# Kernel optimization log

Hardware: AMD Instinct MI355X
Metric: run time of the kernel (lower is better)

## Reference

```python
import jax, jax.numpy as jnp
import numpy as np

B, S, D = 4, 2048, 768   # batch, seq_len, dim_inp
H, E = 12, 64            # num_heads, dim_out (per-head)
LN_EPS = 1e-5


def setup_inputs() -> dict:
    key = jax.random.key(0)
    ks = jax.random.split(key, 12)
    sd = 1.0 / np.sqrt(D)
    x = jax.random.normal(ks[0], (B, S, D), dtype=jnp.float32)
    Wq = jax.random.normal(ks[1], (H, D, E), dtype=jnp.float32) * sd
    bq = jax.random.normal(ks[2], (H, E), dtype=jnp.float32) * 0.02
    Wk = jax.random.normal(ks[3], (H, D, E), dtype=jnp.float32) * sd
    bk = jax.random.normal(ks[4], (H, E), dtype=jnp.float32) * 0.02
    Wv = jax.random.normal(ks[5], (H, D, E), dtype=jnp.float32) * sd
    bv = jax.random.normal(ks[6], (H, E), dtype=jnp.float32) * 0.02
    Wo = jax.random.normal(ks[7], (H * E, D), dtype=jnp.float32) * (1.0 / np.sqrt(H * E))
    bo = jax.random.normal(ks[8], (D,), dtype=jnp.float32) * 0.02
    gamma = jnp.ones((D,), dtype=jnp.float32)
    beta = jnp.zeros((D,), dtype=jnp.float32)
    return {"input_tensor": x, "Wq": Wq, "bq": bq, "Wk": Wk, "bk": bk,
            "Wv": Wv, "bv": bv, "Wo": Wo, "bo": bo, "gamma": gamma, "beta": beta}


def reference(input_tensor, Wq, bq, Wk, bk, Wv, bv, Wo, bo, gamma, beta):
    x = input_tensor  # [B,S,D]
    # all heads at once: [B,H,S,E]
    q = jnp.einsum('bsd,hde->bhse', x, Wq) + bq[None, :, None, :]
    k = jnp.einsum('bsd,hde->bhse', x, Wk) + bk[None, :, None, :]
    v = jnp.einsum('bsd,hde->bhse', x, Wv) + bv[None, :, None, :]
    # NOTE: original divides by sqrt(seq_len) (query.size(1)), not sqrt(head_dim)
    scale = jnp.sqrt(jnp.float32(q.shape[2]))
    scores = jnp.einsum('bhse,bhte->bhst', q, k) / scale  # [B,H,S,S]
    attn = jax.nn.softmax(scores, axis=-1)
    ctx = jnp.einsum('bhst,bhte->bhse', attn, v)          # [B,H,S,E]
    # concat heads along last dim: [B,S,H*E]
    ctx = ctx.transpose(0, 2, 1, 3).reshape(x.shape[0], x.shape[1], -1)
    proj = ctx @ Wo + bo                                   # [B,S,D]
    h = x + proj
    mu = jnp.mean(h, axis=-1, keepdims=True)
    var = jnp.mean(jnp.square(h - mu), axis=-1, keepdims=True)
    y = (h - mu) * jax.lax.rsqrt(var + LN_EPS) * gamma + beta
    return y
```

## Files before the change

### kernel.cpp

```cpp
#include <hip/hip_runtime.h>


typedef __bf16 bf16x8 __attribute__((ext_vector_type(8)));
typedef __bf16 bf16x4 __attribute__((ext_vector_type(4)));
typedef float  f32x4  __attribute__((ext_vector_type(4)));

#define MFMA16(a,b,c) __builtin_amdgcn_mfma_f32_16x16x32_bf16((a),(b),(c),0,0,0)
#define QSCALE2 (0.022097086912079612f * 1.4426950408889634f)

__device__ __forceinline__ void gload16(const void* g, void* l) {
  __builtin_amdgcn_global_load_lds((const __attribute__((address_space(1))) void*)g,
                                   (__attribute__((address_space(3))) void*)l, 16, 0, 0);
}

__global__ __launch_bounds__(256) void pack_kernel(
    const float* __restrict__ x, const float* __restrict__ Wq,
    const float* __restrict__ Wk, const float* __restrict__ Wv,
    const float* __restrict__ Wo,
    __bf16* __restrict__ xb, __bf16* __restrict__ wqkv, __bf16* __restrict__ wot) {
  int tid = blockIdx.x * 256 + threadIdx.x;
  int nth = gridDim.x * 256;
  for (int i = tid; i < 8192 * 768 / 4; i += nth) {
    float4 v = ((const float4*)x)[i];
    bf16x4 o; o[0] = (__bf16)v.x; o[1] = (__bf16)v.y; o[2] = (__bf16)v.z; o[3] = (__bf16)v.w;
    ((bf16x4*)xb)[i] = o;
  }
  for (int i = tid; i < 3 * 768 * 768; i += nth) {
    int n = i / 768, d = i - n * 768;
    int p = n / 768;
    int wn = n - p * 768;
    int h = wn >> 6, e = wn & 63;
    const float* W = (p == 0) ? Wq : (p == 1) ? Wk : Wv;
    wqkv[i] = (__bf16)W[(h * 768 + d) * 64 + e];
  }
  for (int i = tid; i < 768 * 768; i += nth) {
    int n = i / 768, k = i - n * 768;
    wot[i] = (__bf16)Wo[k * 768 + n];
  }
}

#define GEMM_CORE(A_, Bt_, m0_, n0_)                                              \
  __shared__ __bf16 As[128 * 32];                                                 \
  __shared__ __bf16 Bs[128 * 32];                                                 \
  const int tid = threadIdx.x;                                                    \
  const int w = tid >> 6, lane = tid & 63, ln = lane & 15, hi = lane >> 4;        \
  const int wr = w >> 1, wc = w & 1;                                              \
  f32x4 acc[4][4];                                                                \
  {                                                                               \
    f32x4 z = {0.f, 0.f, 0.f, 0.f};                                               \
    _Pragma("unroll") for (int i = 0; i < 4; ++i)                                 \
      _Pragma("unroll") for (int j = 0; j < 4; ++j) acc[i][j] = z;                \
  }                                                                               \
  {                                                                               \
    const int r0 = tid >> 2, cc = (tid & 3) * 8;                                  \
    const __bf16* ga0 = A_ + (size_t)(m0_ + r0) * 768 + cc;                       \
    const __bf16* ga1 = A_ + (size_t)(m0_ + 64 + r0) * 768 + cc;                  \
    const __bf16* gb0 = Bt_ + (size_t)(n0_ + r0) * 768 + cc;                      \
    const __bf16* gb1 = Bt_ + (size_t)(n0_ + 64 + r0) * 768 + cc;                 \
    __bf16* la0 = &As[w * 512];                                                   \
    __bf16* la1 = &As[2048 + w * 512];                                            \
    __bf16* lb0 = &Bs[w * 512];                                                   \
    __bf16* lb1 = &Bs[2048 + w * 512];                                            \
    for (int kt = 0; kt < 24; ++kt) {                                             \
      const int kk = kt * 32;                                                     \
      gload16(ga0 + kk, la0);                                                     \
      gload16(ga1 + kk, la1);                                                     \
      gload16(gb0 + kk, lb0);                                                     \
      gload16(gb1 + kk, lb1);                                                     \
      __syncthreads();                                                            \
      bf16x8 af[4], bfv[4];                                                       \
      _Pragma("unroll") for (int mt = 0; mt < 4; ++mt)                            \
        af[mt] = *(const bf16x8*)&As[(wr * 64 + mt * 16 + ln) * 32 + hi * 8];     \
      _Pragma("unroll") for (int nt = 0; nt < 4; ++nt)                            \
        bfv[nt] = *(const bf16x8*)&Bs[(wc * 64 + nt * 16 + ln) * 32 + hi * 8];    \
      _Pragma("unroll") for (int mt = 0; mt < 4; ++mt)                            \
        _Pragma("unroll") for (int nt = 0; nt < 4; ++nt)                          \
          acc[mt][nt] = MFMA16(af[mt], bfv[nt], acc[mt][nt]);                     \
      __syncthreads();                                                            \
    }                                                                             \
  }

__global__ __launch_bounds__(256) void gemm_qkv(
    const __bf16* __restrict__ A, const __bf16* __restrict__ Bt,
    const float* __restrict__ bq, const float* __restrict__ bk,
    const float* __restrict__ bv,
    __bf16* __restrict__ qb, __bf16* __restrict__ kb, __bf16* __restrict__ vt) {
  const int m0 = blockIdx.y * 128, n0 = blockIdx.x * 128;
  GEMM_CORE(A, Bt, m0, n0)
  const int p = n0 / 768;
  const float* bias = (p == 0) ? bq : (p == 1) ? bk : bv;
  const float sc = (p == 0) ? QSCALE2 : 1.0f;
#pragma unroll
  for (int nt = 0; nt < 4; ++nt) {
    int n = n0 + wc * 64 + nt * 16 + ln;
    int wn = n - p * 768;
    int h = wn >> 6, e = wn & 63;
    float bb = bias[wn];
#pragma unroll
    for (int mt = 0; mt < 4; ++mt) {
      int mrow = m0 + wr * 64 + mt * 16 + hi * 4;
      int b = mrow >> 11, s0 = mrow & 2047;
      if (p == 2) {
        bf16x4 pk;
#pragma unroll
        for (int r = 0; r < 4; ++r) pk[r] = (__bf16)(acc[mt][nt][r] + bb);
        *(bf16x4*)&vt[(((size_t)b * 12 + h) * 64 + e) * 2048 + s0] = pk;
      } else {
        __bf16* dst = (p == 0) ? qb : kb;
#pragma unroll
        for (int r = 0; r < 4; ++r)
          dst[(((size_t)b * 12 + h) * 2048 + s0 + r) * 64 + e] =
              (__bf16)((acc[mt][nt][r] + bb) * sc);
      }
    }
  }
}

__global__ __launch_bounds__(256) void gemm_proj(
    const __bf16* __restrict__ A, const __bf16* __restrict__ Bt,
    const float* __restrict__ bo, const float* __restrict__ xres,
    float* __restrict__ hout) {
  const int m0 = blockIdx.y * 128, n0 = blockIdx.x * 128;
  GEMM_CORE(A, Bt, m0, n0)
#pragma unroll
  for (int nt = 0; nt < 4; ++nt) {
    int n = n0 + wc * 64 + nt * 16 + ln;
    float bb = bo[n];
#pragma unroll
    for (int mt = 0; mt < 4; ++mt) {
      int mrow = m0 + wr * 64 + mt * 16 + hi * 4;
#pragma unroll
      for (int r = 0; r < 4; ++r) {
        size_t idx = (size_t)(mrow + r) * 768 + n;
        hout[idx] = acc[mt][nt][r] + bb + xres[idx];
      }
    }
  }
}

__global__ __launch_bounds__(256) void attn_kernel(
    const __bf16* __restrict__ qb, const __bf16* __restrict__ kb,
    const __bf16* __restrict__ vt, __bf16* __restrict__ ctx) {
  __shared__ __bf16 Kl[64 * 72];
  __shared__ __bf16 Vl[64 * 72];
  __shared__ __bf16 Pl[4][16 * 72];
  const int tid = threadIdx.x;
  const int w = tid >> 6, lane = tid & 63, ln = lane & 15, hi = lane >> 4;
  const int bh = blockIdx.x;
  const int q0 = blockIdx.y * 64;

  const __bf16* qrow = qb + ((size_t)bh * 2048 + q0 + w * 16 + ln) * 64;
  bf16x8 qf0 = *(const bf16x8*)(qrow + hi * 8);
  bf16x8 qf1 = *(const bf16x8*)(qrow + 32 + hi * 8);

  float lsum = 0.f;
  f32x4 cacc[4];
  {
    f32x4 z = {0.f, 0.f, 0.f, 0.f};
#pragma unroll
    for (int eg = 0; eg < 4; ++eg) cacc[eg] = z;
  }

  const int sr = tid >> 3, sc = (tid & 7) * 8;
  const __bf16* gk = kb + ((size_t)bh * 2048 + sr) * 64 + sc;
  const __bf16* gv = vt + ((size_t)bh * 64 + sr) * 2048 + sc;

  bf16x8 k0 = *(const bf16x8*)(gk);
  bf16x8 k1 = *(const bf16x8*)(gk + 32 * 64);
  bf16x8 v0 = *(const bf16x8*)(gv);
  bf16x8 v1 = *(const bf16x8*)(gv + 32 * 2048);

  for (int t = 0; t < 32; ++t) {
    __syncthreads();
    *(bf16x8*)&Kl[sr * 72 + sc] = k0;
    *(bf16x8*)&Kl[(sr + 32) * 72 + sc] = k1;
    *(bf16x8*)&Vl[sr * 72 + sc] = v0;
    *(bf16x8*)&Vl[(sr + 32) * 72 + sc] = v1;
    __syncthreads();
    if (t < 31) {
      const __bf16* nk = gk + (size_t)(t + 1) * 64 * 64;
      const __bf16* nv = gv + (size_t)(t + 1) * 64;
      k0 = *(const bf16x8*)(nk);
      k1 = *(const bf16x8*)(nk + 32 * 64);
      v0 = *(const bf16x8*)(nv);
      v1 = *(const bf16x8*)(nv + 32 * 2048);
    }
#pragma unroll
    for (int tq = 0; tq < 4; ++tq) {
      bf16x8 ka = *(const bf16x8*)&Kl[(tq * 16 + ln) * 72 + hi * 8];
      bf16x8 kb2 = *(const bf16x8*)&Kl[(tq * 16 + ln) * 72 + 32 + hi * 8];
      f32x4 z = {0.f, 0.f, 0.f, 0.f};
      z = MFMA16(ka, qf0, z);
      z = MFMA16(kb2, qf1, z);
      bf16x4 pk;
#pragma unroll
      for (int r = 0; r < 4; ++r) {
        float p = __builtin_amdgcn_exp2f(z[r]);
        lsum += p;
        pk[r] = (__bf16)p;
      }
      *(bf16x4*)&Pl[w][ln * 72 + tq * 16 + hi * 4] = pk;
    }
    bf16x8 pa0 = *(const bf16x8*)&Pl[w][ln * 72 + hi * 8];
    bf16x8 pa1 = *(const bf16x8*)&Pl[w][ln * 72 + 32 + hi * 8];
#pragma unroll
    for (int eg = 0; eg < 4; ++eg) {
      bf16x8 bv0 = *(const bf16x8*)&Vl[(eg * 16 + ln) * 72 + hi * 8];
      bf16x8 bv1 = *(const bf16x8*)&Vl[(eg * 16 + ln) * 72 + 32 + hi * 8];
      cacc[eg] = MFMA16(pa0, bv0, cacc[eg]);
      cacc[eg] = MFMA16(pa1, bv1, cacc[eg]);
    }
  }
  lsum += __shfl_xor(lsum, 16, 64);
  lsum += __shfl_xor(lsum, 32, 64);
  const int b = bh / 12, h = bh - b * 12;
#pragma unroll
  for (int r = 0; r < 4; ++r) {
    float lq = __shfl(lsum, (lane & 48) + hi * 4 + r, 64);
    float rl = 1.0f / lq;
    int qr = q0 + w * 16 + hi * 4 + r;
#pragma unroll
    for (int eg = 0; eg < 4; ++eg)
      ctx[((size_t)b * 2048 + qr) * 768 + h * 64 + eg * 16 + ln] =
          (__bf16)(cacc[eg][r] * rl);
  }
}

__global__ __launch_bounds__(256) void ln_kernel(
    const float* __restrict__ hb, const float* __restrict__ gamma,
    const float* __restrict__ beta, float* __restrict__ out) {
  __shared__ float ssum[4], ssq[4];
  const int row = blockIdx.x, t = threadIdx.x;
  const float* hr = hb + (size_t)row * 768;
  float v0 = hr[t], v1 = hr[t + 256], v2 = hr[t + 512];
  float sum = v0 + v1 + v2;
  float sq = v0 * v0 + v1 * v1 + v2 * v2;
#pragma unroll
  for (int mask = 1; mask < 64; mask <<= 1) {
    sum += __shfl_xor(sum, mask, 64);
    sq += __shfl_xor(sq, mask, 64);
  }
  const int w = t >> 6;
  if ((t & 63) == 0) { ssum[w] = sum; ssq[w] = sq; }
  __syncthreads();
  float s1 = ssum[0] + ssum[1] + ssum[2] + ssum[3];
  float s2 = ssq[0] + ssq[1] + ssq[2] + ssq[3];
  float mu = s1 * (1.0f / 768.0f);
  float var = s2 * (1.0f / 768.0f) - mu * mu;
  float rs = rsqrtf(var + 1e-5f);
  float* orow = out + (size_t)row * 768;
  orow[t]       = (v0 - mu) * rs * gamma[t]       + beta[t];
  orow[t + 256] = (v1 - mu) * rs * gamma[t + 256] + beta[t + 256];
  orow[t + 512] = (v2 - mu) * rs * gamma[t + 512] + beta[t + 512];
}

extern "C" void kernel_launch(void* const* d_in, const int* in_sizes, int n_in,
                              void* d_out, int out_size, void* d_ws, size_t ws_size,
                              hipStream_t stream) {
  const float* x     = (const float*)d_in[0];
  const float* Wq    = (const float*)d_in[1];
  const float* bq    = (const float*)d_in[2];
  const float* Wk    = (const float*)d_in[3];
  const float* bk    = (const float*)d_in[4];
  const float* Wv    = (const float*)d_in[5];
  const float* bv    = (const float*)d_in[6];
  const float* Wo    = (const float*)d_in[7];
  const float* bo    = (const float*)d_in[8];
  const float* gamma = (const float*)d_in[9];
  const float* beta  = (const float*)d_in[10];
  float* out = (float*)d_out;

  char* ws = (char*)d_ws;
  __bf16* xb   = (__bf16*)(ws);
  __bf16* wqkv = (__bf16*)(ws + 12582912);
  __bf16* wot  = (__bf16*)(ws + 16121856);
  __bf16* qb   = (__bf16*)(ws + 17301504);
  __bf16* kb   = (__bf16*)(ws + 29884416);
  __bf16* vt   = (__bf16*)(ws + 42467328);
  __bf16* ctx  = (__bf16*)(ws + 55050240);
  float*  hb   = (float*)(ws + 67633152);

  pack_kernel<<<dim3(1024), dim3(256), 0, stream>>>(x, Wq, Wk, Wv, Wo, xb, wqkv, wot);
  gemm_qkv<<<dim3(18, 64), dim3(256), 0, stream>>>(xb, wqkv, bq, bk, bv, qb, kb, vt);
  attn_kernel<<<dim3(48, 32), dim3(256), 0, stream>>>(qb, kb, vt, ctx);
  gemm_proj<<<dim3(6, 64), dim3(256), 0, stream>>>(ctx, wot, bo, x, hb);
  ln_kernel<<<dim3(8192), dim3(256), 0, stream>>>(hb, gamma, beta, out);
}
```

Before: 194.3 us.

## Rework attention kernel with 32x32 MFMA, async double-buffered LDS, and register P

Rewrites the attention inner loop so each wave handles 32 query rows using 32x32x16 bf16 MFMAs, which halves the grid. K/V tiles are loaded straight into XOR-swizzled LDS with global_load_lds and double-buffered, so one barrier per iteration replaces two. The probability tile stays in registers through cvt_pk_bf16 and permlane32_swap instead of a round trip through LDS. Risks are higher register pressure and fewer blocks per CU, which could lower occupancy.

```diff
diff --git a/kernel.cpp b/kernel.cpp
--- a/kernel.cpp
+++ b/kernel.cpp
@@ -4,8 +4,11 @@
 typedef __bf16 bf16x8 __attribute__((ext_vector_type(8)));
 typedef __bf16 bf16x4 __attribute__((ext_vector_type(4)));
 typedef float  f32x4  __attribute__((ext_vector_type(4)));
+typedef float  f32x16 __attribute__((ext_vector_type(16)));
+typedef unsigned u32x4 __attribute__((ext_vector_type(4)));
 
 #define MFMA16(a,b,c) __builtin_amdgcn_mfma_f32_16x16x32_bf16((a),(b),(c),0,0,0)
+#define MFMA32(a,b,c) __builtin_amdgcn_mfma_f32_32x32x16_bf16((a),(b),(c),0,0,0)
 #define QSCALE2 (0.022097086912079612f * 1.4426950408889634f)
 
 __device__ __forceinline__ void gload16(const void* g, void* l) {
@@ -141,88 +144,114 @@
 __global__ __launch_bounds__(256) void attn_kernel(
     const __bf16* __restrict__ qb, const __bf16* __restrict__ kb,
     const __bf16* __restrict__ vt, __bf16* __restrict__ ctx) {
-  __shared__ __bf16 Kl[64 * 72];
-  __shared__ __bf16 Vl[64 * 72];
-  __shared__ __bf16 Pl[4][16 * 72];
+  __shared__ __align__(16) char lds[32768];
   const int tid = threadIdx.x;
-  const int w = tid >> 6, lane = tid & 63, ln = lane & 15, hi = lane >> 4;
+  const int w = tid >> 6, lane = tid & 63;
+  const int l31 = lane & 31, h = lane >> 5;
   const int bh = blockIdx.x;
-  const int q0 = blockIdx.y * 64;
-
-  const __bf16* qrow = qb + ((size_t)bh * 2048 + q0 + w * 16 + ln) * 64;
-  bf16x8 qf0 = *(const bf16x8*)(qrow + hi * 8);
-  bf16x8 qf1 = *(const bf16x8*)(qrow + 32 + hi * 8);
+  const int q0 = blockIdx.y * 128 + w * 32;
+
+  const int o0 = tid * 16, o1 = o0 + 4096;
+  const int r0s = o0 >> 7, cb0 = o0 & 127;
+  const int r1s = o1 >> 7, cb1 = o1 & 127;
+  const char* kgb = (const char*)(kb + (size_t)bh * 2048 * 64);
+  const char* vgb = (const char*)(vt + (size_t)bh * 64 * 2048);
+  const char* ksrc0 = kgb + r0s * 128 + (cb0 ^ ((r0s & 7) << 4));
+  const char* ksrc1 = kgb + r1s * 128 + (cb1 ^ ((r1s & 7) << 4));
+  const char* vsrc0 = vgb + r0s * 4096 + (cb0 ^ ((r0s & 7) << 4));
+  const char* vsrc1 = vgb + r1s * 4096 + (cb1 ^ ((r1s & 7) << 4));
+  char* kl0 = lds + w * 1024;
+  char* vl0 = lds + 16384 + w * 1024;
+
+#define STAGE(t_, b_) do {                                   \
+    gload16(ksrc0 + (size_t)(t_) * 8192, kl0 + (b_) * 8192); \
+    gload16(ksrc1 + (size_t)(t_) * 8192, kl0 + (b_) * 8192 + 4096); \
+    gload16(vsrc0 + (size_t)(t_) * 128,  vl0 + (b_) * 8192); \
+    gload16(vsrc1 + (size_t)(t_) * 128,  vl0 + (b_) * 8192 + 4096); \
+  } while (0)
+
+  const __bf16* qp = qb + ((size_t)bh * 2048 + q0 + l31) * 64 + h * 8;
+  bf16x8 qf[4];
+#pragma unroll
+  for (int s = 0; s < 4; ++s) qf[s] = *(const bf16x8*)(qp + 16 * s);
+
+  const int swz = (l31 & 7) << 4;
+  const int krd = l31 * 128 + ((h * 16) ^ swz);
+  const int vrd = 16384 + l31 * 128 + ((h * 16) ^ swz);
 
   float lsum = 0.f;
-  f32x4 cacc[4];
-  {
-    f32x4 z = {0.f, 0.f, 0.f, 0.f};
-#pragma unroll
-    for (int eg = 0; eg < 4; ++eg) cacc[eg] = z;
-  }
-
-  const int sr = tid >> 3, sc = (tid & 7) * 8;
-  const __bf16* gk = kb + ((size_t)bh * 2048 + sr) * 64 + sc;
-  const __bf16* gv = vt + ((size_t)bh * 64 + sr) * 2048 + sc;
-
-  bf16x8 k0 = *(const bf16x8*)(gk);
-  bf16x8 k1 = *(const bf16x8*)(gk + 32 * 64);
-  bf16x8 v0 = *(const bf16x8*)(gv);
-  bf16x8 v1 = *(const bf16x8*)(gv + 32 * 2048);
+  f32x16 cacc[2];
+#pragma unroll
+  for (int et = 0; et < 2; ++et)
+#pragma unroll
+    for (int r = 0; r < 16; ++r) cacc[et][r] = 0.f;
+
+  STAGE(0, 0);
+  __syncthreads();
+  int buf = 0;
 
   for (int t = 0; t < 32; ++t) {
+    if (t < 31) STAGE(t + 1, buf ^ 1);
+    const char* kb_l = lds + buf * 8192;
+    u32x4 pau[4];
+#pragma unroll
+    for (int kvt = 0; kvt < 2; ++kvt) {
+      f32x16 sa;
+#pragma unroll
+      for (int r = 0; r < 16; ++r) sa[r] = 0.f;
+      __builtin_amdgcn_s_setprio(1);
+#pragma unroll
+      for (int s = 0; s < 4; ++s) {
+        bf16x8 ka = *(const bf16x8*)(kb_l + ((krd + kvt * 4096) ^ (s * 32)));
+        sa = MFMA32(ka, qf[s], sa);
+      }
+      __builtin_amdgcn_s_setprio(0);
+      unsigned c0, c1, c2, c3, c4, c5, c6, c7;
+#define PKPAIR(dst_, i_)                                                     \
+      {                                                                      \
+        float pa_ = __builtin_amdgcn_exp2f(sa[2 * (i_)]);                    \
+        float pb_ = __builtin_amdgcn_exp2f(sa[2 * (i_) + 1]);                \
+        lsum += pa_ + pb_;                                                   \
+        asm("v_cvt_pk_bf16_f32 %0, %1, %2" : "=v"(dst_) : "v"(pa_), "v"(pb_)); \
+      }
+      PKPAIR(c0, 0) PKPAIR(c1, 1) PKPAIR(c2, 2) PKPAIR(c3, 3)
+      PKPAIR(c4, 4) PKPAIR(c5, 5) PKPAIR(c6, 6) PKPAIR(c7, 7)
+#undef PKPAIR
+      asm("v_permlane32_swap_b32 %0, %1" : "+v"(c0), "+v"(c2));
+      asm("v_permlane32_swap_b32 %0, %1" : "+v"(c1), "+v"(c3));
+      asm("v_permlane32_swap_b32 %0, %1" : "+v"(c4), "+v"(c6));
+      asm("v_permlane32_swap_b32 %0, %1" : "+v"(c5), "+v"(c7));
+      pau[2 * kvt][0] = c0; pau[2 * kvt][1] = c1;
+      pau[2 * kvt][2] = c2; pau[2 * kvt][3] = c3;
+      pau[2 * kvt + 1][0] = c4; pau[2 * kvt + 1][1] = c5;
+      pau[2 * kvt + 1][2] = c6; pau[2 * kvt + 1][3] = c7;
+    }
+    const char* vb_l = lds + buf * 8192;
+    __builtin_amdgcn_s_setprio(1);
+#pragma unroll
+    for (int ks = 0; ks < 4; ++ks) {
+      bf16x8 paf = __builtin_bit_cast(bf16x8, pau[ks]);
+      bf16x8 bv0 = *(const bf16x8*)(vb_l + ((vrd + 0 * 4096) ^ (ks * 32)));
+      bf16x8 bv1 = *(const bf16x8*)(vb_l + ((vrd + 1 * 4096) ^ (ks * 32)));
+      cacc[0] = MFMA32(paf, bv0, cacc[0]);
+      cacc[1] = MFMA32(paf, bv1, cacc[1]);
+    }
+    __builtin_amdgcn_s_setprio(0);
     __syncthreads();
-    *(bf16x8*)&Kl[sr * 72 + sc] = k0;
-    *(bf16x8*)&Kl[(sr + 32) * 72 + sc] = k1;
-    *(bf16x8*)&Vl[sr * 72 + sc] = v0;
-    *(bf16x8*)&Vl[(sr + 32) * 72 + sc] = v1;
-    __syncthreads();
-    if (t < 31) {
-      const __bf16* nk = gk + (size_t)(t + 1) * 64 * 64;
-      const __bf16* nv = gv + (size_t)(t + 1) * 64;
-      k0 = *(const bf16x8*)(nk);
-      k1 = *(const bf16x8*)(nk + 32 * 64);
-      v0 = *(const bf16x8*)(nv);
-      v1 = *(const bf16x8*)(nv + 32 * 2048);
-    }
-#pragma unroll
-    for (int tq = 0; tq < 4; ++tq) {
-      bf16x8 ka = *(const bf16x8*)&Kl[(tq * 16 + ln) * 72 + hi * 8];
-      bf16x8 kb2 = *(const bf16x8*)&Kl[(tq * 16 + ln) * 72 + 32 + hi * 8];
-      f32x4 z = {0.f, 0.f, 0.f, 0.f};
-      z = MFMA16(ka, qf0, z);
-      z = MFMA16(kb2, qf1, z);
-      bf16x4 pk;
-#pragma unroll
-      for (int r = 0; r < 4; ++r) {
-        float p = __builtin_amdgcn_exp2f(z[r]);
-        lsum += p;
-        pk[r] = (__bf16)p;
-      }
-      *(bf16x4*)&Pl[w][ln * 72 + tq * 16 + hi * 4] = pk;
-    }
-    bf16x8 pa0 = *(const bf16x8*)&Pl[w][ln * 72 + hi * 8];
-    bf16x8 pa1 = *(const bf16x8*)&Pl[w][ln * 72 + 32 + hi * 8];
-#pragma unroll
-    for (int eg = 0; eg < 4; ++eg) {
-      bf16x8 bv0 = *(const bf16x8*)&Vl[(eg * 16 + ln) * 72 + hi * 8];
-      bf16x8 bv1 = *(const bf16x8*)&Vl[(eg * 16 + ln) * 72 + 32 + hi * 8];
-      cacc[eg] = MFMA16(pa0, bv0, cacc[eg]);
-      cacc[eg] = MFMA16(pa1, bv1, cacc[eg]);
-    }
-  }
-  lsum += __shfl_xor(lsum, 16, 64);
+    buf ^= 1;
+  }
+#undef STAGE
+
   lsum += __shfl_xor(lsum, 32, 64);
-  const int b = bh / 12, h = bh - b * 12;
-#pragma unroll
-  for (int r = 0; r < 4; ++r) {
-    float lq = __shfl(lsum, (lane & 48) + hi * 4 + r, 64);
-    float rl = 1.0f / lq;
-    int qr = q0 + w * 16 + hi * 4 + r;
-#pragma unroll
-    for (int eg = 0; eg < 4; ++eg)
-      ctx[((size_t)b * 2048 + qr) * 768 + h * 64 + eg * 16 + ln] =
-          (__bf16)(cacc[eg][r] * rl);
+  float inv = 1.0f / lsum;
+  const int b = bh / 12, hh = bh - b * 12;
+#pragma unroll
+  for (int r = 0; r < 16; ++r) {
+    const int ql = (r & 3) + 8 * (r >> 2) + 4 * h;
+    float rl = __shfl(inv, ql, 64);
+    size_t base = ((size_t)b * 2048 + q0 + ql) * 768 + hh * 64 + l31;
+    ctx[base]      = (__bf16)(cacc[0][r] * rl);
+    ctx[base + 32] = (__bf16)(cacc[1][r] * rl);
   }
 }
 
@@ -282,7 +311,7 @@
 
   pack_kernel<<<dim3(1024), dim3(256), 0, stream>>>(x, Wq, Wk, Wv, Wo, xb, wqkv, wot);
   gemm_qkv<<<dim3(18, 64), dim3(256), 0, stream>>>(xb, wqkv, bq, bk, bv, qb, kb, vt);
-  attn_kernel<<<dim3(48, 32), dim3(256), 0, stream>>>(qb, kb, vt, ctx);
+  attn_kernel<<<dim3(48, 16), dim3(256), 0, stream>>>(qb, kb, vt, ctx);
   gemm_proj<<<dim3(6, 64), dim3(256), 0, stream>>>(ctx, wot, bo, x, hb);
   ln_kernel<<<dim3(8192), dim3(256), 0, stream>>>(hb, gamma, beta, out);
 }
```

After: 172.9 us. -11.0%, faster.
